# Optimization experiments

Hardware: AMD Instinct MI355X
Metric: run time of the kernel (lower is better)

## Reference

```python
import jax, jax.numpy as jnp
import numpy as np

B, T, D = 4, 4096, 1024


def setup_inputs() -> dict:
    key = jax.random.key(0)
    ks = jax.random.split(key, 10)
    scale = 1.0 / np.sqrt(D)
    x = jax.random.normal(ks[0], (B, T, D), jnp.float32)
    last_x = jnp.zeros((D,), jnp.float32)
    last_num = jnp.zeros((D,), jnp.float32)
    last_den = jnp.zeros((D,), jnp.float32)
    time_decay = jax.random.normal(ks[1], (D,), jnp.float32) * 0.1
    time_first = jax.random.normal(ks[2], (D,), jnp.float32) * 0.1
    time_mix_k = jax.random.uniform(ks[3], (1, 1, D), jnp.float32)
    time_mix_v = jax.random.uniform(ks[4], (1, 1, D), jnp.float32)
    time_mix_r = jax.random.uniform(ks[5], (1, 1, D), jnp.float32)
    Wk = jax.random.normal(ks[6], (D, D), jnp.float32) * scale
    Wv = jax.random.normal(ks[7], (D, D), jnp.float32) * scale
    Wr = jax.random.normal(ks[8], (D, D), jnp.float32) * scale
    Wo = jax.random.normal(ks[9], (D, D), jnp.float32) * scale
    return {"x": x, "last_x": last_x, "last_num": last_num, "last_den": last_den,
            "time_decay": time_decay, "time_first": time_first,
            "time_mix_k": time_mix_k, "time_mix_v": time_mix_v, "time_mix_r": time_mix_r,
            "Wk": Wk, "Wv": Wv, "Wr": Wr, "Wo": Wo}


def reference(x, last_x, last_num, last_den, time_decay, time_first,
              time_mix_k, time_mix_v, time_mix_r, Wk, Wv, Wr, Wo):
    # token-shift lerps against the incoming state (broadcast over B, T)
    k = jnp.einsum('btd,ed->bte', x * time_mix_k + last_x * (1.0 - time_mix_k), Wk)
    v = jnp.einsum('btd,ed->bte', x * time_mix_v + last_x * (1.0 - time_mix_v), Wv)
    r = jnp.einsum('btd,ed->bte', x * time_mix_r + last_x * (1.0 - time_mix_r), Wr)
    # WKV numerics, exactly as the original (no extra stabilization)
    efk = jnp.exp(time_first + k)          # exp(time_first + k), [B,T,D]
    wkv = (last_num + efk * v) / (last_den + efk)
    rwkv = jax.nn.sigmoid(r) * wkv
    decay = jnp.exp(-jnp.exp(time_decay))  # [D]
    ek = jnp.exp(k)
    num = decay * last_num + ek * v
    den = decay * last_den + ek
    out = jnp.einsum('btd,ed->bte', rwkv, Wo)
    return out, x[..., -1, :], num[..., -1, :], den[..., -1, :]
```

## Files before the change

### kernel.cpp

```cpp
#include <hip/hip_runtime.h>
#include <cstdint>
#include <cstddef>

constexpr int DD = 1024;
constexpr int TT = 4096;
constexpr int BB = 4;
constexpr int MM = BB * TT;

typedef __bf16 bf16x8 __attribute__((ext_vector_type(8)));
typedef float  f32x4  __attribute__((ext_vector_type(4)));

__device__ __forceinline__ unsigned short f2bf(float f) {
  union { float f; uint32_t u; } c; c.f = f;
  uint32_t r = (c.u + 0x7FFFu + ((c.u >> 16) & 1u)) >> 16;
  return (unsigned short)r;
}

__device__ __forceinline__ float fast_rcp(float x) {
  return __builtin_amdgcn_rcpf(x);
}

__device__ __forceinline__ void async_ld16(const unsigned short* g, unsigned short* lds_dst) {
  __builtin_amdgcn_global_load_lds(
      (const __attribute__((address_space(1))) void*)g,
      (__attribute__((address_space(3))) void*)lds_dst,
      16, 0, 0);
}

#define VWAIT(n) asm volatile("s_waitcnt vmcnt(" #n ")" ::: "memory")
#define LWAIT0() asm volatile("s_waitcnt lgkmcnt(0)" ::: "memory")
#define SB()     __builtin_amdgcn_sched_barrier(0)

__device__ __forceinline__ int swzb(int b) { return b ^ (((b >> 9) & 1) << 5); }

__global__ void prep_all(const float* __restrict__ Wk, const float* __restrict__ Wv,
                         const float* __restrict__ Wr, const float* __restrict__ Wo,
                         const float* __restrict__ tmk, const float* __restrict__ tmv,
                         const float* __restrict__ tmr,
                         const float* __restrict__ last_x,
                         const float4* __restrict__ x,
                         unsigned short* __restrict__ wz,
                         unsigned short* __restrict__ wo,
                         float* __restrict__ bias,
                         ushort4* __restrict__ xb,
                         float4* __restrict__ out_xlast) {
  if (blockIdx.x < 1024) {
    int w = (blockIdx.x * 256 + threadIdx.x) >> 6;
    int lane = threadIdx.x & 63;
    int z = w >> 10;
    int e = w & (DD - 1);
    const float* W  = (z == 0) ? Wk  : (z == 1) ? Wv  : (z == 2) ? Wr : Wo;
    const float* tm = (z == 0) ? tmk : (z == 1) ? tmv : tmr;
    unsigned short* dst = (z < 3) ? (wz + (size_t)z * DD * DD + (size_t)e * DD)
                                  : (wo + (size_t)e * DD);
    float s = 0.f;
#pragma unroll
    for (int j = 0; j < 4; ++j) {
      int d = j * 256 + lane * 4;
      float4 wv4 = *(const float4*)(W + (size_t)e * DD + d);
      if (z < 3) {
        float4 t4 = *(const float4*)(tm + d);
        float4 l4 = *(const float4*)(last_x + d);
        s += l4.x * (1.f - t4.x) * wv4.x + l4.y * (1.f - t4.y) * wv4.y +
             l4.z * (1.f - t4.z) * wv4.z + l4.w * (1.f - t4.w) * wv4.w;
        wv4.x *= t4.x; wv4.y *= t4.y; wv4.z *= t4.z; wv4.w *= t4.w;
      }
      ushort4 o;
      o.x = f2bf(wv4.x); o.y = f2bf(wv4.y); o.z = f2bf(wv4.z); o.w = f2bf(wv4.w);
      *(ushort4*)(dst + d) = o;
    }
    if (z < 3) {
      for (int off = 32; off; off >>= 1) s += __shfl_down(s, off, 64);
      if (lane == 0) bias[z * DD + e] = s;
    }
  } else {
    int i = (blockIdx.x - 1024) * 256 + threadIdx.x;
    float4 v = x[i];
    ushort4 o;
    o.x = f2bf(v.x); o.y = f2bf(v.y); o.z = f2bf(v.z); o.w = f2bf(v.w);
    xb[i] = o;
    int m = i >> 8;
    if ((m & (TT - 1)) == (TT - 1)) {
      int b = m >> 12;
      out_xlast[b * 256 + (i & 255)] = v;
    }
  }
}

__global__ __launch_bounds__(256, 2) void gemm_kvr(
    const unsigned short* __restrict__ A,
    const unsigned short* __restrict__ Wz,
    const float* __restrict__ bias,
    const float* __restrict__ time_first, const float* __restrict__ time_decay,
    const float* __restrict__ last_num, const float* __restrict__ last_den,
    unsigned short* __restrict__ rwkv,
    float* __restrict__ out_num, float* __restrict__ out_den) {
  __shared__ unsigned short lA[2][128 * 32];
  __shared__ unsigned short lB[2][3][64 * 32];
  const int tid  = threadIdx.x;
  const int lane = tid & 63;
  const int wave = tid >> 6;

  const int id  = blockIdx.y * gridDim.x + blockIdx.x;
  const int xcd = id & 7;
  const int s   = id >> 3;
  const int m0 = (xcd * 16 + (s >> 4)) * 128;
  const int n0 = (s & 15) * 64;

  const int wm = (wave >> 1) * 64;
  const int wn = (wave & 1) * 32;

  f32x4 acc[3][4][2] = {};

  const int fr_row = lane & 15;
  const int fr_kb  = (lane >> 4) * 16;
  const int srow = tid >> 2;
  const int scol = (tid & 3) * 8;

  for (int k0 = 0; k0 < DD; k0 += 64) {
    __syncthreads();
#pragma unroll
    for (int h = 0; h < 2; ++h) {
      int kk = k0 + h * 32;
#pragma unroll
      for (int it = 0; it < 2; ++it) {
        int cc  = it * 256 + tid;
        int row = cc >> 2;
        async_ld16(A + (size_t)(m0 + row) * DD + (kk + scol),
                   lA[h] + (size_t)(it * 256 + wave * 64) * 8);
      }
#pragma unroll
      for (int z = 0; z < 3; ++z) {
        async_ld16(Wz + (size_t)z * DD * DD + (size_t)(n0 + srow) * DD + (kk + scol),
                   lB[h][z] + (size_t)(wave * 64) * 8);
      }
    }
    __syncthreads();

#pragma unroll
    for (int h = 0; h < 2; ++h) {
      bf16x8 af[4], bfr[3][2];
#pragma unroll
      for (int i = 0; i < 4; ++i)
        af[i] = *(const bf16x8*)((const char*)lA[h] + ((wm + i * 16 + fr_row) * 64 + fr_kb));
#pragma unroll
      for (int z = 0; z < 3; ++z)
#pragma unroll
        for (int j = 0; j < 2; ++j)
          bfr[z][j] = *(const bf16x8*)((const char*)lB[h][z] + ((wn + j * 16 + fr_row) * 64 + fr_kb));

#pragma unroll
      for (int mi = 0; mi < 4; ++mi)
#pragma unroll
        for (int z = 0; z < 3; ++z)
#pragma unroll
          for (int ni = 0; ni < 2; ++ni)
            acc[z][mi][ni] = __builtin_amdgcn_mfma_f32_16x16x32_bf16(
                af[mi], bfr[z][ni], acc[z][mi][ni], 0, 0, 0);
    }
  }

  const int crow = (lane >> 4) * 4;
  const int ccol = lane & 15;
#pragma unroll
  for (int ni = 0; ni < 2; ++ni) {
    int gnz = n0 + wn + ni * 16 + ccol;
    float bk = bias[gnz], bv = bias[DD + gnz], br = bias[2 * DD + gnz];
    float tf = time_first[gnz];
    float ln = last_num[gnz], ld = last_den[gnz];
    float dec = __expf(-__expf(time_decay[gnz]));
#pragma unroll
    for (int mi = 0; mi < 4; ++mi) {
#pragma unroll
      for (int r = 0; r < 4; ++r) {
        int gm = m0 + wm + mi * 16 + crow + r;
        float kk = acc[0][mi][ni][r] + bk;
        float vv = acc[1][mi][ni][r] + bv;
        float rr = acc[2][mi][ni][r] + br;
        float efk = __expf(tf + kk);
        float wkv = (ln + efk * vv) * fast_rcp(ld + efk);
        float sr  = fast_rcp(1.0f + __expf(-rr));
        rwkv[(size_t)gm * DD + gnz] = f2bf(sr * wkv);
        if ((gm & (TT - 1)) == (TT - 1)) {
          int b = gm >> 12;
          float ek = __expf(kk);
          out_num[b * DD + gnz] = dec * ln + ek * vv;
          out_den[b * DD + gnz] = dec * ld + ek;
        }
      }
    }
  }
}

__global__ __launch_bounds__(512, 2) void gemm_bt256(
    const unsigned short* __restrict__ A,
    const unsigned short* __restrict__ Bw,
    float* __restrict__ Cf,
    int M, int N, int K) {
  __shared__ __align__(1024) unsigned short sA[4][256 * 32];
  __shared__ __align__(1024) unsigned short sB[4][256 * 32];
  const int tid  = threadIdx.x;
  const int lane = tid & 63;
  const int wave = tid >> 6;

  const int id  = blockIdx.y * gridDim.x + blockIdx.x;
  const int xcd = id & 7;
  const int s   = id >> 3;
  const int m0 = (xcd * 8 + (s >> 2)) * 256;
  const int n0 = (s & 3) * 256;

  const int wm = (wave >> 2) * 128;
  const int wn = (wave & 3) * 64;
  const int fr = lane & 15;
  const int fq = lane >> 4;

  int phA[8], phB[4];
#pragma unroll
  for (int mi = 0; mi < 8; ++mi)
    phA[mi] = swzb((wm + mi * 16 + fr) * 64 + fq * 16);
#pragma unroll
  for (int ni = 0; ni < 4; ++ni)
    phB[ni] = swzb((wn + ni * 16 + fr) * 64 + fq * 16);

  size_t aSrc[2], bSrc[2]; int dPl[2];
#pragma unroll
  for (int u = 0; u < 2; ++u) {
    int plane = u * 8 + wave;
    dPl[u] = plane * 1024;
    int pb = plane * 1024 + lane * 16;
    int lq = swzb(pb);
    int r = lq >> 6, cb = lq & 63;
    aSrc[u] = (size_t)(m0 + r) * K + (cb >> 1);
    bSrc[u] = (size_t)(n0 + r) * K + (cb >> 1);
  }
  auto stageA = [&](int slot, int t) {
    const int kk = t * 32;
#pragma unroll
    for (int u = 0; u < 2; ++u)
      async_ld16(A + aSrc[u] + kk, (unsigned short*)((char*)sA[slot] + dPl[u]));
  };
  auto stageB = [&](int slot, int t) {
    const int kk = t * 32;
#pragma unroll
    for (int u = 0; u < 2; ++u)
      async_ld16(Bw + bSrc[u] + kk, (unsigned short*)((char*)sB[slot] + dPl[u]));
  };

  f32x4 acc[8][4] = {};
  const int nt = K >> 5;

  stageA(0, 0); stageB(0, 0);
  stageA(1, 1); stageB(1, 1);
  stageA(2, 2); stageB(2, 2);
  VWAIT(8); SB();
  __builtin_amdgcn_s_barrier();

#pragma unroll 1
  for (int t = 0; t < nt; ++t) {
    const int slot = t & 3;

    bf16x8 af0[4], bf[4];
#pragma unroll
    for (int mi = 0; mi < 4; ++mi)
      af0[mi] = *(const bf16x8*)((const char*)sA[slot] + phA[mi]);
#pragma unroll
    for (int ni = 0; ni < 4; ++ni)
      bf[ni] = *(const bf16x8*)((const char*)sB[slot] + phB[ni]);
    if (t < nt - 3) stageA((t + 3) & 3, t + 3);
    __builtin_amdgcn_s_barrier();
    LWAIT0(); SB();
    __builtin_amdgcn_s_setprio(1);
#pragma unroll
    for (int mi = 0; mi < 4; ++mi)
#pragma unroll
      for (int ni = 0; ni < 4; ++ni)
        acc[mi][ni] = __builtin_amdgcn_mfma_f32_16x16x32_bf16(
            af0[mi], bf[ni], acc[mi][ni], 0, 0, 0);
    __builtin_amdgcn_s_setprio(0);
    __builtin_amdgcn_s_barrier();

    bf16x8 af1[4];
#pragma unroll
    for (int mi = 0; mi < 4; ++mi)
      af1[mi] = *(const bf16x8*)((const char*)sA[slot] + phA[4 + mi]);
    if (t < nt - 3) stageB((t + 3) & 3, t + 3);
    __builtin_amdgcn_s_barrier();
    LWAIT0(); SB();
    __builtin_amdgcn_s_setprio(1);
#pragma unroll
    for (int mi = 0; mi < 4; ++mi)
#pragma unroll
      for (int ni = 0; ni < 4; ++ni)
        acc[4 + mi][ni] = __builtin_amdgcn_mfma_f32_16x16x32_bf16(
            af1[mi], bf[ni], acc[4 + mi][ni], 0, 0, 0);
    __builtin_amdgcn_s_setprio(0);

    if (t < nt - 1) {
      if (t < nt - 3)       VWAIT(8);
      else if (t == nt - 3) VWAIT(4);
      else                  VWAIT(0);
      SB();
      __builtin_amdgcn_s_barrier();
    }
  }

  const int crow = fq * 4;
  const int ccol = fr;
#pragma unroll
  for (int mi = 0; mi < 8; ++mi) {
#pragma unroll
    for (int ni = 0; ni < 4; ++ni) {
      int gn = n0 + wn + ni * 16 + ccol;
#pragma unroll
      for (int r = 0; r < 4; ++r) {
        int gm = m0 + wm + mi * 16 + crow + r;
        Cf[(size_t)gm * N + gn] = acc[mi][ni][r];
      }
    }
  }
}

extern "C" void kernel_launch(void* const* d_in, const int* in_sizes, int n_in,
                              void* d_out, int out_size, void* d_ws, size_t ws_size,
                              hipStream_t stream) {
  const float* x          = (const float*)d_in[0];
  const float* last_x     = (const float*)d_in[1];
  const float* last_num   = (const float*)d_in[2];
  const float* last_den   = (const float*)d_in[3];
  const float* time_decay = (const float*)d_in[4];
  const float* time_first = (const float*)d_in[5];
  const float* tmk        = (const float*)d_in[6];
  const float* tmv        = (const float*)d_in[7];
  const float* tmr        = (const float*)d_in[8];
  const float* Wk         = (const float*)d_in[9];
  const float* Wv         = (const float*)d_in[10];
  const float* Wr         = (const float*)d_in[11];
  const float* Wo         = (const float*)d_in[12];

  float* out       = (float*)d_out;
  float* out_xlast = out + (size_t)MM * DD;
  float* out_num   = out_xlast + BB * DD;
  float* out_den   = out_num + BB * DD;

  char* ws = (char*)d_ws;
  unsigned short* xb   = (unsigned short*)ws;
  unsigned short* wz   = (unsigned short*)(ws + 33554432);
  unsigned short* wo   = (unsigned short*)(ws + 39845888);
  float*          bias = (float*)(ws + 41943040);
  unsigned short* rwkv = (unsigned short*)(ws + 41955328);

  prep_all<<<1024 + MM * DD / 4 / 256, 256, 0, stream>>>(
      Wk, Wv, Wr, Wo, tmk, tmv, tmr, last_x, (const float4*)x,
      wz, wo, bias, (ushort4*)xb, (float4*)out_xlast);

  gemm_kvr<<<dim3(DD / 64, MM / 128), 256, 0, stream>>>(
      xb, wz, bias, time_first, time_decay, last_num, last_den,
      rwkv, out_num, out_den);

  gemm_bt256<<<dim3(DD / 256, MM / 256), 512, 0, stream>>>(
      rwkv, wo, out, MM, DD, DD);
}
```

Measured before the change: 293.2 us.

## Split KVR GEMM and run half the rows on a pipelined swizzled kernel

```diff
diff --git a/kernel.cpp b/kernel.cpp
--- a/kernel.cpp
+++ b/kernel.cpp
@@ -87,79 +87,12 @@
   }
 }
 
-__global__ __launch_bounds__(256, 2) void gemm_kvr(
-    const unsigned short* __restrict__ A,
-    const unsigned short* __restrict__ Wz,
-    const float* __restrict__ bias,
-    const float* __restrict__ time_first, const float* __restrict__ time_decay,
-    const float* __restrict__ last_num, const float* __restrict__ last_den,
-    unsigned short* __restrict__ rwkv,
+__device__ __forceinline__ void wkv_epilogue(
+    f32x4 (&acc)[3][4][2], int m0, int n0, int wm, int wn, int lane,
+    const float* __restrict__ bias, const float* __restrict__ time_first,
+    const float* __restrict__ time_decay, const float* __restrict__ last_num,
+    const float* __restrict__ last_den, unsigned short* __restrict__ rwkv,
     float* __restrict__ out_num, float* __restrict__ out_den) {
-  __shared__ unsigned short lA[2][128 * 32];
-  __shared__ unsigned short lB[2][3][64 * 32];
-  const int tid  = threadIdx.x;
-  const int lane = tid & 63;
-  const int wave = tid >> 6;
-
-  const int id  = blockIdx.y * gridDim.x + blockIdx.x;
-  const int xcd = id & 7;
-  const int s   = id >> 3;
-  const int m0 = (xcd * 16 + (s >> 4)) * 128;
-  const int n0 = (s & 15) * 64;
-
-  const int wm = (wave >> 1) * 64;
-  const int wn = (wave & 1) * 32;
-
-  f32x4 acc[3][4][2] = {};
-
-  const int fr_row = lane & 15;
-  const int fr_kb  = (lane >> 4) * 16;
-  const int srow = tid >> 2;
-  const int scol = (tid & 3) * 8;
-
-  for (int k0 = 0; k0 < DD; k0 += 64) {
-    __syncthreads();
-#pragma unroll
-    for (int h = 0; h < 2; ++h) {
-      int kk = k0 + h * 32;
-#pragma unroll
-      for (int it = 0; it < 2; ++it) {
-        int cc  = it * 256 + tid;
-        int row = cc >> 2;
-        async_ld16(A + (size_t)(m0 + row) * DD + (kk + scol),
-                   lA[h] + (size_t)(it * 256 + wave * 64) * 8);
-      }
-#pragma unroll
-      for (int z = 0; z < 3; ++z) {
-        async_ld16(Wz + (size_t)z * DD * DD + (size_t)(n0 + srow) * DD + (kk + scol),
-                   lB[h][z] + (size_t)(wave * 64) * 8);
-      }
-    }
-    __syncthreads();
-
-#pragma unroll
-    for (int h = 0; h < 2; ++h) {
-      bf16x8 af[4], bfr[3][2];
-#pragma unroll
-      for (int i = 0; i < 4; ++i)
-        af[i] = *(const bf16x8*)((const char*)lA[h] + ((wm + i * 16 + fr_row) * 64 + fr_kb));
-#pragma unroll
-      for (int z = 0; z < 3; ++z)
-#pragma unroll
-        for (int j = 0; j < 2; ++j)
-          bfr[z][j] = *(const bf16x8*)((const char*)lB[h][z] + ((wn + j * 16 + fr_row) * 64 + fr_kb));
-
-#pragma unroll
-      for (int mi = 0; mi < 4; ++mi)
-#pragma unroll
-        for (int z = 0; z < 3; ++z)
-#pragma unroll
-          for (int ni = 0; ni < 2; ++ni)
-            acc[z][mi][ni] = __builtin_amdgcn_mfma_f32_16x16x32_bf16(
-                af[mi], bfr[z][ni], acc[z][mi][ni], 0, 0, 0);
-    }
-  }
-
   const int crow = (lane >> 4) * 4;
   const int ccol = lane & 15;
 #pragma unroll
@@ -192,6 +125,229 @@
   }
 }
 
+__global__ __launch_bounds__(256, 2) void gemm_kvr_a(
+    const unsigned short* __restrict__ A, const unsigned short* __restrict__ Wz,
+    const float* __restrict__ bias,
+    const float* __restrict__ time_first, const float* __restrict__ time_decay,
+    const float* __restrict__ last_num, const float* __restrict__ last_den,
+    unsigned short* __restrict__ rwkv,
+    float* __restrict__ out_num, float* __restrict__ out_den) {
+  __shared__ unsigned short lA[2][128 * 32];
+  __shared__ unsigned short lB[2][3][64 * 32];
+  const int tid  = threadIdx.x;
+  const int lane = tid & 63;
+  const int wave = tid >> 6;
+
+  const int id  = blockIdx.y * gridDim.x + blockIdx.x;
+  const int xcd = id & 7;
+  const int s   = id >> 3;
+  const int m0 = (xcd * 8 + (s >> 4)) * 128;
+  const int n0 = (s & 15) * 64;
+
+  const int wm = (wave >> 1) * 64;
+  const int wn = (wave & 1) * 32;
+
+  f32x4 acc[3][4][2] = {};
+
+  const int fr_row = lane & 15;
+  const int fr_kb  = (lane >> 4) * 16;
+  const int srow = tid >> 2;
+  const int scol = (tid & 3) * 8;
+
+  for (int k0 = 0; k0 < DD; k0 += 64) {
+    __syncthreads();
+#pragma unroll
+    for (int h = 0; h < 2; ++h) {
+      int kk = k0 + h * 32;
+#pragma unroll
+      for (int it = 0; it < 2; ++it) {
+        int cc  = it * 256 + tid;
+        int row = cc >> 2;
+        async_ld16(A + (size_t)(m0 + row) * DD + (kk + scol),
+                   lA[h] + (size_t)(it * 256 + wave * 64) * 8);
+      }
+#pragma unroll
+      for (int z = 0; z < 3; ++z) {
+        async_ld16(Wz + (size_t)z * DD * DD + (size_t)(n0 + srow) * DD + (kk + scol),
+                   lB[h][z] + (size_t)(wave * 64) * 8);
+      }
+    }
+    __syncthreads();
+
+#pragma unroll
+    for (int h = 0; h < 2; ++h) {
+      bf16x8 af[4], bfr[3][2];
+#pragma unroll
+      for (int i = 0; i < 4; ++i)
+        af[i] = *(const bf16x8*)((const char*)lA[h] + ((wm + i * 16 + fr_row) * 64 + fr_kb));
+#pragma unroll
+      for (int z = 0; z < 3; ++z)
+#pragma unroll
+        for (int j = 0; j < 2; ++j)
+          bfr[z][j] = *(const bf16x8*)((const char*)lB[h][z] + ((wn + j * 16 + fr_row) * 64 + fr_kb));
+
+#pragma unroll
+      for (int mi = 0; mi < 4; ++mi)
+#pragma unroll
+        for (int z = 0; z < 3; ++z)
+#pragma unroll
+          for (int ni = 0; ni < 2; ++ni)
+            acc[z][mi][ni] = __builtin_amdgcn_mfma_f32_16x16x32_bf16(
+                af[mi], bfr[z][ni], acc[z][mi][ni], 0, 0, 0);
+    }
+  }
+
+  wkv_epilogue(acc, m0, n0, wm, wn, lane, bias, time_first, time_decay,
+               last_num, last_den, rwkv, out_num, out_den);
+}
+
+__global__ __launch_bounds__(512, 2) void gemm_kvr_b(
+    const unsigned short* __restrict__ A, const unsigned short* __restrict__ Wz,
+    const float* __restrict__ bias,
+    const float* __restrict__ time_first, const float* __restrict__ time_decay,
+    const float* __restrict__ last_num, const float* __restrict__ last_den,
+    unsigned short* __restrict__ rwkv,
+    float* __restrict__ out_num, float* __restrict__ out_den) {
+  __shared__ __align__(1024) unsigned short sA[4][256 * 32];
+  __shared__ __align__(1024) unsigned short sB[4][3 * 64 * 32];
+  const int tid  = threadIdx.x;
+  const int lane = tid & 63;
+  const int wave = tid >> 6;
+
+  const int id  = blockIdx.y * gridDim.x + blockIdx.x;
+  const int xcd = id & 7;
+  const int s   = id >> 3;
+  const int m0 = 8192 + (xcd * 4 + (s >> 4)) * 256;
+  const int n0 = (s & 15) * 64;
+
+  const int wm = (wave >> 1) * 64;
+  const int wn = (wave & 1) * 32;
+  const int fr = lane & 15;
+  const int fq = lane >> 4;
+
+  int phA[4], phB[3][2];
+#pragma unroll
+  for (int m = 0; m < 4; ++m)
+    phA[m] = swzb((wm + m * 16 + fr) * 64 + fq * 16);
+#pragma unroll
+  for (int z = 0; z < 3; ++z)
+#pragma unroll
+    for (int n = 0; n < 2; ++n)
+      phB[z][n] = swzb(z * 4096 + (wn + n * 16 + fr) * 64 + fq * 16);
+
+  size_t aSrc[2]; int aDst[2];
+#pragma unroll
+  for (int u = 0; u < 2; ++u) {
+    int plane = wave * 2 + u;
+    aDst[u] = plane * 1024;
+    int pb = plane * 1024 + lane * 16;
+    int lq = swzb(pb);
+    int r = lq >> 6, cb = lq & 63;
+    aSrc[u] = (size_t)(m0 + r) * DD + (cb >> 1);
+  }
+  size_t bSrc0, bSrc1; int bDst0, bDst1;
+  {
+    int plane = (wave < 4) ? (wave * 2) : (8 + (wave - 4));
+    bDst0 = plane * 1024;
+    int pb = plane * 1024 + lane * 16;
+    int lq = swzb(pb);
+    int r = lq >> 6, cb = lq & 63;
+    int z = r >> 6, zr = r & 63;
+    bSrc0 = (size_t)z * DD * DD + (size_t)(n0 + zr) * DD + (cb >> 1);
+  }
+  {
+    int plane = wave * 2 + 1;
+    bDst1 = plane * 1024;
+    int pb = plane * 1024 + lane * 16;
+    int lq = swzb(pb);
+    int r = lq >> 6, cb = lq & 63;
+    int z = r >> 6, zr = r & 63;
+    bSrc1 = (size_t)z * DD * DD + (size_t)(n0 + zr) * DD + (cb >> 1);
+  }
+
+  auto stageA = [&](int slot, int t) {
+    const int kk = t * 32;
+#pragma unroll
+    for (int u = 0; u < 2; ++u)
+      async_ld16(A + aSrc[u] + kk, (unsigned short*)((char*)sA[slot] + aDst[u]));
+  };
+  auto stageB = [&](int slot, int t) {
+    const int kk = t * 32;
+    async_ld16(Wz + bSrc0 + kk, (unsigned short*)((char*)sB[slot] + bDst0));
+    if (wave < 4)
+      async_ld16(Wz + bSrc1 + kk, (unsigned short*)((char*)sB[slot] + bDst1));
+  };
+
+  f32x4 acc[3][4][2] = {};
+
+  stageA(0, 0); stageB(0, 0);
+  stageA(1, 1); stageB(1, 1);
+  stageA(2, 2); stageB(2, 2);
+  if (wave < 4) VWAIT(8); else VWAIT(6);
+  SB();
+  __builtin_amdgcn_s_barrier();
+
+#pragma unroll 1
+  for (int t = 0; t < 32; ++t) {
+    const int slot = t & 3;
+
+    bf16x8 af[4], b0[2], b1[2];
+#pragma unroll
+    for (int m = 0; m < 4; ++m)
+      af[m] = *(const bf16x8*)((const char*)sA[slot] + phA[m]);
+#pragma unroll
+    for (int n = 0; n < 2; ++n) {
+      b0[n] = *(const bf16x8*)((const char*)sB[slot] + phB[0][n]);
+      b1[n] = *(const bf16x8*)((const char*)sB[slot] + phB[1][n]);
+    }
+    if (t < 29) stageA((t + 3) & 3, t + 3);
+    __builtin_amdgcn_s_barrier();
+    LWAIT0(); SB();
+    __builtin_amdgcn_s_setprio(1);
+#pragma unroll
+    for (int mi = 0; mi < 4; ++mi)
+#pragma unroll
+      for (int ni = 0; ni < 2; ++ni)
+        acc[0][mi][ni] = __builtin_amdgcn_mfma_f32_16x16x32_bf16(
+            af[mi], b0[ni], acc[0][mi][ni], 0, 0, 0);
+#pragma unroll
+    for (int mi = 0; mi < 4; ++mi)
+#pragma unroll
+      for (int ni = 0; ni < 2; ++ni)
+        acc[1][mi][ni] = __builtin_amdgcn_mfma_f32_16x16x32_bf16(
+            af[mi], b1[ni], acc[1][mi][ni], 0, 0, 0);
+    __builtin_amdgcn_s_setprio(0);
+    __builtin_amdgcn_s_barrier();
+
+    bf16x8 b2[2];
+#pragma unroll
+    for (int n = 0; n < 2; ++n)
+      b2[n] = *(const bf16x8*)((const char*)sB[slot] + phB[2][n]);
+    if (t < 29) stageB((t + 3) & 3, t + 3);
+    __builtin_amdgcn_s_barrier();
+    LWAIT0(); SB();
+    __builtin_amdgcn_s_setprio(1);
+#pragma unroll
+    for (int mi = 0; mi < 4; ++mi)
+#pragma unroll
+      for (int ni = 0; ni < 2; ++ni)
+        acc[2][mi][ni] = __builtin_amdgcn_mfma_f32_16x16x32_bf16(
+            af[mi], b2[ni], acc[2][mi][ni], 0, 0, 0);
+    __builtin_amdgcn_s_setprio(0);
+
+    if (t < 31) {
+      if (t < 29)       { if (wave < 4) VWAIT(8); else VWAIT(6); }
+      else if (t == 29) { if (wave < 4) VWAIT(4); else VWAIT(3); }
+      else              { VWAIT(0); }
+      SB();
+      __builtin_amdgcn_s_barrier();
+    }
+  }
+
+  wkv_epilogue(acc, m0, n0, wm, wn, lane, bias, time_first, time_decay,
+               last_num, last_den, rwkv, out_num, out_den);
+}
+
 __global__ __launch_bounds__(512, 2) void gemm_bt256(
     const unsigned short* __restrict__ A,
     const unsigned short* __restrict__ Bw,
@@ -353,10 +509,14 @@
       Wk, Wv, Wr, Wo, tmk, tmv, tmr, last_x, (const float4*)x,
       wz, wo, bias, (ushort4*)xb, (float4*)out_xlast);
 
-  gemm_kvr<<<dim3(DD / 64, MM / 128), 256, 0, stream>>>(
+  gemm_kvr_a<<<dim3(16, 64), 256, 0, stream>>>(
       xb, wz, bias, time_first, time_decay, last_num, last_den,
       rwkv, out_num, out_den);
 
+  gemm_kvr_b<<<dim3(16, 32), 512, 0, stream>>>(
+      xb, wz, bias, time_first, time_decay, last_num, last_den,
+      rwkv, out_num, out_den);
+
   gemm_bt256<<<dim3(DD / 256, MM / 256), 512, 0, stream>>>(
       rwkv, wo, out, MM, DD, DD);
 }
```

Result: slower. 305.1 us (+4.1%).
